# Performance work log

Hardware: AMD Instinct MI355X
Metric: run time of the kernel (lower is better)

The kernel has to match this reference:

```python
import jax, jax.numpy as jnp
import numpy as np

B, C, H, W = 32, 256, 56, 56
WS = 7            # window size (grid/dilated windows)
NH = 4            # num heads = C // dim_head
DH = 64           # dim_head
CMID = 256        # dim_mid = dim_in * exp_ratio
EPS = 1e-5


def _depthwise(x, w):
    # x: (b, C, h, w), w: (C, 1, k, k), 'same' padding, groups=C
    return jax.lax.conv_general_dilated(
        x, w, window_strides=(1, 1), padding='SAME',
        feature_group_count=x.shape[1],
        dimension_numbers=('NCHW', 'OIHW', 'NCHW'))


def setup_inputs() -> dict:
    key = jax.random.key(0)
    ks = jax.random.split(key, 12)
    return {
        'x': jax.random.normal(ks[0], (B, C, H, W), jnp.float32),
        'bn_gamma': jnp.ones((C,), jnp.float32),
        'bn_beta': jnp.zeros((C,), jnp.float32),
        'bn_mean': jnp.zeros((C,), jnp.float32),
        'bn_var': jnp.ones((C,), jnp.float32),
        'w_qk': jax.random.normal(ks[1], (2 * C, C), jnp.float32) * 0.05,
        'w_v': jax.random.normal(ks[2], (CMID, C), jnp.float32) * 0.05,
        'w_conv3': jax.random.normal(ks[3], (CMID, 1, 3, 3), jnp.float32) * 0.1,
        'w_conv5': jax.random.normal(ks[4], (CMID, 1, 5, 5), jnp.float32) * 0.1,
        'w_conv7': jax.random.normal(ks[5], (CMID, 1, 7, 7), jnp.float32) * 0.1,
        'attn_w': jax.random.uniform(ks[6], (1, CMID, 1, 1), jnp.float32),
        'c3_w': jax.random.uniform(ks[7], (1, CMID, 1, 1), jnp.float32),
        'c5_w': jax.random.uniform(ks[8], (1, CMID, 1, 1), jnp.float32),
        'c7_w': jax.random.uniform(ks[9], (1, CMID, 1, 1), jnp.float32),
        'w_proj': jax.random.normal(ks[10], (C, CMID), jnp.float32) * 0.05,
    }


def reference(x, bn_gamma, bn_beta, bn_mean, bn_var, w_qk, w_v,
              w_conv3, w_conv5, w_conv7, attn_w, c3_w, c5_w, c7_w, w_proj):
    shortcut = x
    # BatchNorm2d (eval mode, running stats)
    g = (bn_gamma / jnp.sqrt(bn_var + EPS))[None, :, None, None]
    x = (x - bn_mean[None, :, None, None]) * g + bn_beta[None, :, None, None]

    Bc, Cc, Hc, Wc = x.shape
    n1, n2 = Hc // WS, Wc // WS
    # grid/dilated windowing: 'b c (h1 n1) (w1 n2) -> (b n1 n2) c h1 w1'
    xw = (x.reshape(Bc, Cc, WS, n1, WS, n2)
           .transpose(0, 3, 5, 1, 2, 4)
           .reshape(Bc * n1 * n2, Cc, WS, WS))
    b = xw.shape[0]
    hw = WS * WS

    # qk 1x1 conv -> split into per-head q, k: (b, nh, hw, dh)
    qk = jnp.einsum('oc,bchw->bohw', w_qk, xw).reshape(b, 2, NH, DH, hw)
    q = qk[:, 0].transpose(0, 1, 3, 2)
    k = qk[:, 1].transpose(0, 1, 3, 2)

    # v 1x1 conv (attn_pre=False: attention over projected v)
    v = jnp.einsum('oc,bchw->bohw', w_v, xw)  # (b, CMID, ws, ws)
    vh = v.reshape(b, NH, CMID // NH, hw).transpose(0, 1, 3, 2)

    scale = 1.0 / jnp.sqrt(jnp.asarray(DH, x.dtype))
    attn = jax.nn.softmax(jnp.einsum('bnqd,bnkd->bnqk', q, k) * scale, axis=-1)
    x_spa = (jnp.einsum('bnqk,bnkd->bnqd', attn, vh)
             .transpose(0, 1, 3, 2).reshape(b, CMID, WS, WS))

    # multi-scale depthwise conv branch + weighted fusion + residual
    c3 = _depthwise(v, w_conv3)
    c5 = _depthwise(v, w_conv5)
    c7 = _depthwise(v, w_conv7)
    xc = x_spa * attn_w + c3 * c3_w + c5 * c5_w + c7 * c7_w + v

    # unwindow: '(b n1 n2) c h1 w1 -> b c (h1 n1) (w1 n2)'
    x = (xc.reshape(Bc, n1, n2, CMID, WS, WS)
           .transpose(0, 3, 4, 1, 5, 2)
           .reshape(Bc, CMID, Hc, Wc))

    # output 1x1 projection + residual (drop/drop_path are 0)
    x = jnp.einsum('oc,bchw->bohw', w_proj, x)
    return shortcut + x
```

## Files before the change

kernel.cpp:

```cpp
#include <hip/hip_runtime.h>
#include <cstddef>
#include <cstdint>

typedef short bf16x8 __attribute__((ext_vector_type(8)));
typedef float f32x4 __attribute__((ext_vector_type(4)));

#define MFMA16(a, b, c) __builtin_amdgcn_mfma_f32_16x16x32_bf16((a), (b), (c), 0, 0, 0)

__device__ __forceinline__ unsigned short f2bf(float f) {
  unsigned u = __float_as_uint(f);
  u = (u + 0x7FFFu + ((u >> 16) & 1u)) >> 16;
  return (unsigned short)u;
}
__device__ __forceinline__ float bf2f(unsigned short h) {
  return __uint_as_float(((unsigned)h) << 16);
}

__global__ void wprep(const float* __restrict__ bn_g, const float* __restrict__ bn_b,
                      const float* __restrict__ bn_m, const float* __restrict__ bn_v,
                      const float* __restrict__ w_qk, const float* __restrict__ w_v,
                      const float* __restrict__ w_proj,
                      const float* __restrict__ w3, const float* __restrict__ w5,
                      const float* __restrict__ w7,
                      unsigned short* __restrict__ Wqk, unsigned short* __restrict__ Wv,
                      unsigned short* __restrict__ Wp,
                      float* __restrict__ bqk, float* __restrict__ bv,
                      float* __restrict__ w3T, float* __restrict__ w5T,
                      float* __restrict__ w7T) {
  int blk = blockIdx.x, t = threadIdx.x;
  if (blk == 4) {
    for (int idx = t; idx < 21248; idx += 256) {
      if (idx < 2304) {
        int k2 = idx >> 8, c = idx & 255;
        w3T[idx] = w3[c * 9 + k2];
      } else if (idx < 8704) {
        int i = idx - 2304;
        int k2 = i >> 8, c = i & 255;
        w5T[i] = w5[c * 25 + k2];
      } else {
        int i = idx - 8704;
        int k2 = i >> 8, c = i & 255;
        w7T[i] = w7[c * 49 + k2];
      }
    }
    return;
  }
  int o = blk * 256 + t;
  if (o < 512) {
    float scale = (o < 256) ? 0.125f : 1.0f;
    float bias = 0.f;
    for (int c = 0; c < 256; ++c) {
      float g = bn_g[c] / sqrtf(bn_v[c] + 1e-5f);
      float be = bn_b[c] - bn_m[c] * g;
      float wv = w_qk[o * 256 + c];
      bias += wv * be;
      Wqk[o * 256 + c] = f2bf(wv * g * scale);
    }
    bqk[o] = bias * scale;
  } else if (o < 768) {
    int oo = o - 512;
    float bias = 0.f;
    for (int c = 0; c < 256; ++c) {
      float g = bn_g[c] / sqrtf(bn_v[c] + 1e-5f);
      float be = bn_b[c] - bn_m[c] * g;
      float wv = w_v[oo * 256 + c];
      bias += wv * be;
      Wv[oo * 256 + c] = f2bf(wv * g);
    }
    bv[oo] = bias;
  } else {
    int oo = o - 768;
    for (int c = 0; c < 256; ++c) Wp[oo * 256 + c] = f2bf(w_proj[oo * 256 + c]);
  }
}

__global__ __launch_bounds__(256) void xpose(const float* __restrict__ x,
                                             unsigned short* __restrict__ xT) {
  __shared__ float tile[64 * 68];
  int blk = blockIdx.x;
  int bb = blk / 196;
  int rem = blk - bb * 196;
  int cblk = rem / 49;
  int pblk = rem - cblk * 49;
  int t = threadIdx.x;
  {
    int r = t >> 2, seg = t & 3;
    const float* src = x + (size_t)bb * 802816 + (size_t)(cblk * 64 + r) * 3136 +
                       pblk * 64 + seg * 16;
    float4 v0 = ((const float4*)src)[0];
    float4 v1 = ((const float4*)src)[1];
    float4 v2 = ((const float4*)src)[2];
    float4 v3 = ((const float4*)src)[3];
    float* td = tile + r * 68 + seg * 16;
    td[0] = v0.x; td[1] = v0.y; td[2] = v0.z; td[3] = v0.w;
    td[4] = v1.x; td[5] = v1.y; td[6] = v1.z; td[7] = v1.w;
    td[8] = v2.x; td[9] = v2.y; td[10] = v2.z; td[11] = v2.w;
    td[12] = v3.x; td[13] = v3.y; td[14] = v3.z; td[15] = v3.w;
  }
  __syncthreads();
  {
    int p = t >> 2, cs = t & 3;
    alignas(16) unsigned short tmp[16];
#pragma unroll
    for (int u = 0; u < 16; ++u) tmp[u] = f2bf(tile[(cs * 16 + u) * 68 + p]);
    unsigned short* dst = xT + (size_t)(bb * 3136 + pblk * 64 + p) * 256 +
                          cblk * 64 + cs * 16;
    ((uint4*)dst)[0] = *(const uint4*)(tmp);
    ((uint4*)dst)[1] = *(const uint4*)(tmp + 8);
  }
}

__global__ __launch_bounds__(512, 2) void k2_win(
    const unsigned short* __restrict__ xT, const unsigned short* __restrict__ Wqk,
    const unsigned short* __restrict__ Wv, const float* __restrict__ bqk,
    const float* __restrict__ bv, const float* __restrict__ w3T,
    const float* __restrict__ w5T, const float* __restrict__ w7T,
    const float* __restrict__ aw, const float* __restrict__ c3w,
    const float* __restrict__ c5w, const float* __restrict__ c7w,
    unsigned short* __restrict__ xcT) {
  extern __shared__ char smem[];
  unsigned short* v_lds = (unsigned short*)smem;
  unsigned short* xw = (unsigned short*)(smem + 36864);
  unsigned short* q_lds = (unsigned short*)(smem + 62736);
  unsigned short* k_lds = (unsigned short*)(smem + 81168);
  unsigned short* Sb = (unsigned short*)(smem + 99600);
  float* spa = (float*)(smem + 118032);

  const int tid = threadIdx.x;
  const int l = tid & 63;
  const int w = tid >> 6;
  const int l15 = l & 15;
  const int lg = l >> 4;
  const int blk = blockIdx.x;
  const int bb = blk >> 6, i1 = (blk >> 3) & 7, i2 = blk & 7;

  for (int idx = tid; idx < 1568; idx += 512) {
    int r = idx >> 5, seg = idx & 31;
    int h1 = (r * 9363) >> 16;
    int w1 = r - h1 * 7;
    int pix = bb * 3136 + (h1 * 8 + i1) * 56 + w1 * 8 + i2;
    uint4 d = *(const uint4*)(xT + (size_t)pix * 256 + seg * 8);
    *(uint4*)(xw + r * 264 + seg * 8) = d;
  }
  __syncthreads();

  {
    f32x4 acc[2][4];
#pragma unroll
    for (int mf = 0; mf < 2; ++mf)
#pragma unroll
      for (int nt = 0; nt < 4; ++nt) acc[mf][nt] = (f32x4){0.f, 0.f, 0.f, 0.f};
#pragma unroll 2
    for (int ks = 0; ks < 8; ++ks) {
      bf16x8 a0 = *(const bf16x8*)(Wv + (w * 32 + l15) * 256 + ks * 32 + lg * 8);
      bf16x8 a1 = *(const bf16x8*)(Wv + (w * 32 + 16 + l15) * 256 + ks * 32 + lg * 8);
      bf16x8 b[4];
#pragma unroll
      for (int nt = 0; nt < 4; ++nt) {
        int j = nt * 16 + l15;
        if (j > 48) j = 48;
        b[nt] = *(const bf16x8*)(xw + j * 264 + ks * 32 + lg * 8);
      }
#pragma unroll
      for (int nt = 0; nt < 4; ++nt) {
        acc[0][nt] = MFMA16(a0, b[nt], acc[0][nt]);
        acc[1][nt] = MFMA16(a1, b[nt], acc[1][nt]);
      }
    }
#pragma unroll
    for (int mf = 0; mf < 2; ++mf)
#pragma unroll
      for (int ri = 0; ri < 4; ++ri) {
        int c = w * 32 + mf * 16 + lg * 4 + ri;
        float bvv = bv[c];
#pragma unroll
        for (int nt = 0; nt < 4; ++nt) {
          int p = nt * 16 + l15;
          v_lds[c * 72 + p] = f2bf(acc[mf][nt][ri] + bvv);
        }
      }
  }
  __syncthreads();

  for (int hp = 0; hp < 2; ++hp) {
    const int hs = w >> 2;
    const int sub = w & 3;
    const int h = hp * 2 + hs;

    {
      int obase = (sub < 2) ? (h * 64 + sub * 32) : (256 + h * 64 + (sub & 1) * 32);
      f32x4 acc[2][4];
#pragma unroll
      for (int mf = 0; mf < 2; ++mf)
#pragma unroll
        for (int nt = 0; nt < 4; ++nt) acc[mf][nt] = (f32x4){0.f, 0.f, 0.f, 0.f};
#pragma unroll 2
      for (int ks = 0; ks < 8; ++ks) {
        bf16x8 a0 = *(const bf16x8*)(Wqk + (obase + l15) * 256 + ks * 32 + lg * 8);
        bf16x8 a1 = *(const bf16x8*)(Wqk + (obase + 16 + l15) * 256 + ks * 32 + lg * 8);
        bf16x8 b[4];
#pragma unroll
        for (int nt = 0; nt < 4; ++nt) {
          int j = nt * 16 + l15;
          if (j > 48) j = 48;
          b[nt] = *(const bf16x8*)(xw + j * 264 + ks * 32 + lg * 8);
        }
#pragma unroll
        for (int nt = 0; nt < 4; ++nt) {
          acc[0][nt] = MFMA16(a0, b[nt], acc[0][nt]);
          acc[1][nt] = MFMA16(a1, b[nt], acc[1][nt]);
        }
      }
      unsigned short* dst = ((sub < 2) ? q_lds : k_lds) + hs * 4608;
      int dbase = (sub & 1) * 32;
#pragma unroll
      for (int mf = 0; mf < 2; ++mf)
#pragma unroll
        for (int ri = 0; ri < 4; ++ri) {
          float bias = bqk[obase + mf * 16 + lg * 4 + ri];
          int d = dbase + mf * 16 + lg * 4 + ri;
#pragma unroll
          for (int nt = 0; nt < 4; ++nt) {
            int p = nt * 16 + l15;
            dst[p * 72 + d] = f2bf(acc[mf][nt][ri] + bias);
          }
        }
    }
    __syncthreads();

    {
      f32x4 s[4];
#pragma unroll
      for (int nt = 0; nt < 4; ++nt) s[nt] = (f32x4){0.f, 0.f, 0.f, 0.f};
#pragma unroll
      for (int ks = 0; ks < 2; ++ks) {
        bf16x8 a = *(const bf16x8*)(q_lds + hs * 4608 + (sub * 16 + l15) * 72 +
                                    ks * 32 + lg * 8);
        bf16x8 b[4];
#pragma unroll
        for (int nt = 0; nt < 4; ++nt)
          b[nt] = *(const bf16x8*)(k_lds + hs * 4608 + (nt * 16 + l15) * 72 +
                                   ks * 32 + lg * 8);
#pragma unroll
        for (int nt = 0; nt < 4; ++nt) s[nt] = MFMA16(a, b[nt], s[nt]);
      }
#pragma unroll
      for (int ri = 0; ri < 4; ++ri) {
        float s0 = s[0][ri], s1 = s[1][ri], s2 = s[2][ri], s3v = s[3][ri];
        if (l15 != 0) s3v = -1e30f;
        float m = fmaxf(fmaxf(s0, s1), fmaxf(s2, s3v));
        m = fmaxf(m, __shfl_xor(m, 1));
        m = fmaxf(m, __shfl_xor(m, 2));
        m = fmaxf(m, __shfl_xor(m, 4));
        m = fmaxf(m, __shfl_xor(m, 8));
        float e0 = __expf(s0 - m), e1 = __expf(s1 - m);
        float e2 = __expf(s2 - m), e3 = __expf(s3v - m);
        float sum = e0 + e1 + e2 + e3;
        sum += __shfl_xor(sum, 1);
        sum += __shfl_xor(sum, 2);
        sum += __shfl_xor(sum, 4);
        sum += __shfl_xor(sum, 8);
        float inv = 1.f / sum;
        int row = sub * 16 + lg * 4 + ri;
        unsigned short* sb = Sb + hs * 4608 + row * 72 + l15;
        sb[0] = f2bf(e0 * inv);
        sb[16] = f2bf(e1 * inv);
        sb[32] = f2bf(e2 * inv);
        sb[48] = f2bf(e3 * inv);
      }
    }
    __syncthreads();

    {
      f32x4 acc[4];
#pragma unroll
      for (int nt = 0; nt < 4; ++nt) acc[nt] = (f32x4){0.f, 0.f, 0.f, 0.f};
#pragma unroll
      for (int ks = 0; ks < 2; ++ks) {
        bf16x8 a = *(const bf16x8*)(Sb + hs * 4608 + (sub * 16 + l15) * 72 +
                                    ks * 32 + lg * 8);
        bf16x8 b[4];
#pragma unroll
        for (int nt = 0; nt < 4; ++nt)
          b[nt] = *(const bf16x8*)(v_lds + (h * 64 + nt * 16 + l15) * 72 +
                                   ks * 32 + lg * 8);
#pragma unroll
        for (int nt = 0; nt < 4; ++nt) acc[nt] = MFMA16(a, b[nt], acc[nt]);
      }
#pragma unroll
      for (int nt = 0; nt < 4; ++nt)
#pragma unroll
        for (int ri = 0; ri < 4; ++ri) {
          int p = sub * 16 + lg * 4 + ri;
          if (p < 49) spa[hs * 3328 + (nt * 16 + l15) * 52 + p] = acc[nt][ri];
        }
    }
    __syncthreads();

    {
      int cl = ((w & 1) << 6) + l;
      int c = hp * 128 + cl;
      int hs2 = cl >> 6, dp = cl & 63;
      const float* spaC = spa + hs2 * 3328 + dp * 52;
      float awc = aw[c], c3c = c3w[c], c5c = c5w[c], c7c = c7w[c];
      float W3[9], W5[25], W7[49];
#pragma unroll
      for (int k2 = 0; k2 < 9; ++k2) W3[k2] = w3T[k2 * 256 + c];
#pragma unroll
      for (int k2 = 0; k2 < 25; ++k2) W5[k2] = w5T[k2 * 256 + c];
#pragma unroll
      for (int k2 = 0; k2 < 49; ++k2) W7[k2] = w7T[k2 * 256 + c];
#pragma unroll
      for (int pass = 0; pass < 2; ++pass) {
        int hr = (w >> 1) + pass * 4;
        if (hr <= 6) {
          float vr[7][7];
#pragma unroll
          for (int dy = -3; dy <= 3; ++dy) {
            int ry = hr + dy;
            if ((unsigned)ry < 7u) {
#pragma unroll
              for (int cc = 0; cc < 7; ++cc)
                vr[dy + 3][cc] = bf2f(v_lds[c * 72 + ry * 7 + cc]);
            }
          }
          float sp[7];
#pragma unroll
          for (int ww = 0; ww < 7; ++ww) sp[ww] = spaC[hr * 7 + ww];
#pragma unroll
          for (int ww = 0; ww < 7; ++ww) {
            float s3a = 0.f, s5a = 0.f, s7a = 0.f;
#pragma unroll
            for (int dy = -3; dy <= 3; ++dy) {
              if ((unsigned)(hr + dy) < 7u) {
#pragma unroll
                for (int dx = -3; dx <= 3; ++dx) {
                  int cc = ww + dx;
                  if (cc >= 0 && cc < 7) {
                    float vv = vr[dy + 3][cc];
                    s7a = fmaf(W7[(dy + 3) * 7 + dx + 3], vv, s7a);
                    if (dy >= -2 && dy <= 2 && dx >= -2 && dx <= 2)
                      s5a = fmaf(W5[(dy + 2) * 5 + dx + 2], vv, s5a);
                    if (dy >= -1 && dy <= 1 && dx >= -1 && dx <= 1)
                      s3a = fmaf(W3[(dy + 1) * 3 + dx + 1], vv, s3a);
                  }
                }
              }
            }
            float val = sp[ww] * awc + s3a * c3c + s5a * c5c + s7a * c7c + vr[3][ww];
            int pixp = bb * 3136 + (hr * 8 + i1) * 56 + ww * 8 + i2;
            xcT[(size_t)pixp * 256 + c] = f2bf(val);
          }
        }
      }
    }
    __syncthreads();
  }
}

__global__ __launch_bounds__(256) void k3_proj(const unsigned short* __restrict__ Wp,
                                               const unsigned short* __restrict__ xcT,
                                               const float* __restrict__ x,
                                               float* __restrict__ out) {
  const int tid = threadIdx.x, l = tid & 63, w = tid >> 6;
  const int l15 = l & 15, lg = l >> 4;
  const int blk = blockIdx.x;
  f32x4 acc[4][4];
#pragma unroll
  for (int mf = 0; mf < 4; ++mf)
#pragma unroll
    for (int nf = 0; nf < 4; ++nf) acc[mf][nf] = (f32x4){0.f, 0.f, 0.f, 0.f};
#pragma unroll 2
  for (int ks = 0; ks < 8; ++ks) {
    bf16x8 a[4], b[4];
#pragma unroll
    for (int mf = 0; mf < 4; ++mf)
      a[mf] = *(const bf16x8*)(Wp + (w * 64 + mf * 16 + l15) * 256 + ks * 32 + lg * 8);
#pragma unroll
    for (int nf = 0; nf < 4; ++nf)
      b[nf] = *(const bf16x8*)(xcT + (size_t)(blk * 64 + nf * 16 + l15) * 256 +
                               ks * 32 + lg * 8);
#pragma unroll
    for (int mf = 0; mf < 4; ++mf)
#pragma unroll
      for (int nf = 0; nf < 4; ++nf) acc[mf][nf] = MFMA16(a[mf], b[nf], acc[mf][nf]);
  }
  int bb = (blk * 64) / 3136;
  int loc0 = blk * 64 - bb * 3136;
#pragma unroll
  for (int mf = 0; mf < 4; ++mf)
#pragma unroll
    for (int nf = 0; nf < 4; ++nf)
#pragma unroll
      for (int ri = 0; ri < 4; ++ri) {
        int o = w * 64 + mf * 16 + lg * 4 + ri;
        int ploc = loc0 + nf * 16 + l15;
        size_t addr = (size_t)bb * 802816 + (size_t)o * 3136 + ploc;
        out[addr] = x[addr] + acc[mf][nf][ri];
      }
}

extern "C" void kernel_launch(void* const* d_in, const int* in_sizes, int n_in,
                              void* d_out, int out_size, void* d_ws, size_t ws_size,
                              hipStream_t stream) {
  const float* x = (const float*)d_in[0];
  const float* bn_g = (const float*)d_in[1];
  const float* bn_b = (const float*)d_in[2];
  const float* bn_m = (const float*)d_in[3];
  const float* bn_v = (const float*)d_in[4];
  const float* w_qk = (const float*)d_in[5];
  const float* w_v = (const float*)d_in[6];
  const float* w3 = (const float*)d_in[7];
  const float* w5 = (const float*)d_in[8];
  const float* w7 = (const float*)d_in[9];
  const float* aw = (const float*)d_in[10];
  const float* c3w = (const float*)d_in[11];
  const float* c5w = (const float*)d_in[12];
  const float* c7w = (const float*)d_in[13];
  const float* w_pr = (const float*)d_in[14];
  float* out = (float*)d_out;
  char* ws = (char*)d_ws;

  unsigned short* Wqk = (unsigned short*)ws;
  unsigned short* Wv = (unsigned short*)(ws + 262144);
  unsigned short* Wp = (unsigned short*)(ws + 393216);
  float* bqk = (float*)(ws + 524288);
  float* bv = (float*)(ws + 526336);
  float* w3T = (float*)(ws + 527360);
  float* w5T = (float*)(ws + 536576);
  float* w7T = (float*)(ws + 562176);
  unsigned short* xT = (unsigned short*)(ws + 1048576);
  unsigned short* xcT = (unsigned short*)(ws + 52428800);

  wprep<<<5, 256, 0, stream>>>(bn_g, bn_b, bn_m, bn_v, w_qk, w_v, w_pr, w3, w5, w7,
                               Wqk, Wv, Wp, bqk, bv, w3T, w5T, w7T);
  xpose<<<6272, 256, 0, stream>>>(x, xT);
  hipFuncSetAttribute(reinterpret_cast<const void*>(k2_win),
                      hipFuncAttributeMaxDynamicSharedMemorySize, 144656);
  k2_win<<<2048, 512, 144656, stream>>>(xT, Wqk, Wv, bqk, bv, w3T, w5T, w7T, aw, c3w,
                                        c5w, c7w, xcT);
  k3_proj<<<1568, 256, 0, stream>>>(Wp, xcT, x, out);
}
```

Before: 418.7 us.

## Process one head per iteration to shrink LDS and double k2 occupancy

Restructures the window kernel so each iteration handles one head. The V projection for that head is computed alongside Q/K in the same loop rather than as a separate full-width stage. This cuts dynamic shared memory from about 145 KB to about 74 KB and raises launch bounds to 4 blocks per SM, aiming for more resident waves to hide latency. In exchange there are more sequential barriers per block, and half the waves sit idle in the softmax stage and one wave in the depthwise stage. Register pressure under the tighter launch bound could cause spills in the depthwise-conv section.

```diff
diff --git a/kernel.cpp b/kernel.cpp
--- a/kernel.cpp
+++ b/kernel.cpp
@@ -110,7 +110,7 @@
   }
 }
 
-__global__ __launch_bounds__(512, 2) void k2_win(
+__global__ __launch_bounds__(512, 4) void k2_win(
     const unsigned short* __restrict__ xT, const unsigned short* __restrict__ Wqk,
     const unsigned short* __restrict__ Wv, const float* __restrict__ bqk,
     const float* __restrict__ bv, const float* __restrict__ w3T,
@@ -119,85 +119,41 @@
     const float* __restrict__ c5w, const float* __restrict__ c7w,
     unsigned short* __restrict__ xcT) {
   extern __shared__ char smem[];
-  unsigned short* v_lds = (unsigned short*)smem;
-  unsigned short* xw = (unsigned short*)(smem + 36864);
-  unsigned short* q_lds = (unsigned short*)(smem + 62736);
-  unsigned short* k_lds = (unsigned short*)(smem + 81168);
-  unsigned short* Sb = (unsigned short*)(smem + 99600);
-  float* spa = (float*)(smem + 118032);
+  unsigned short* xw = (unsigned short*)smem;
+  unsigned short* v_lds = (unsigned short*)(smem + 25872);
+  unsigned short* q_lds = (unsigned short*)(smem + 33152);
+  unsigned short* k_lds = (unsigned short*)(smem + 42368);
+  unsigned short* Sb = (unsigned short*)(smem + 51584);
+  float* spa = (float*)(smem + 60800);
 
   const int tid = threadIdx.x;
-  const int l = tid & 63;
-  const int w = tid >> 6;
-  const int l15 = l & 15;
-  const int lg = l >> 4;
+  const int l = tid & 63, w = tid >> 6, l15 = l & 15, lg = l >> 4;
   const int blk = blockIdx.x;
   const int bb = blk >> 6, i1 = (blk >> 3) & 7, i2 = blk & 7;
 
   for (int idx = tid; idx < 1568; idx += 512) {
     int r = idx >> 5, seg = idx & 31;
-    int h1 = (r * 9363) >> 16;
-    int w1 = r - h1 * 7;
+    int h1 = (r * 9363) >> 16, w1 = r - h1 * 7;
     int pix = bb * 3136 + (h1 * 8 + i1) * 56 + w1 * 8 + i2;
-    uint4 d = *(const uint4*)(xT + (size_t)pix * 256 + seg * 8);
-    *(uint4*)(xw + r * 264 + seg * 8) = d;
-  }
+    *(uint4*)(xw + r * 264 + seg * 8) =
+        *(const uint4*)(xT + (size_t)pix * 256 + seg * 8);
+  }
+  if (tid < 8) v_lds[64 * 56 + tid] = 0;
   __syncthreads();
 
-  {
-    f32x4 acc[2][4];
-#pragma unroll
-    for (int mf = 0; mf < 2; ++mf)
-#pragma unroll
-      for (int nt = 0; nt < 4; ++nt) acc[mf][nt] = (f32x4){0.f, 0.f, 0.f, 0.f};
-#pragma unroll 2
-    for (int ks = 0; ks < 8; ++ks) {
-      bf16x8 a0 = *(const bf16x8*)(Wv + (w * 32 + l15) * 256 + ks * 32 + lg * 8);
-      bf16x8 a1 = *(const bf16x8*)(Wv + (w * 32 + 16 + l15) * 256 + ks * 32 + lg * 8);
-      bf16x8 b[4];
+  for (int h = 0; h < 4; ++h) {
+    {
+      const bool isq = (w < 4);
+      const int wt = isq ? w : (w - 4);
+      const int obase = isq ? (h * 64 + wt * 16) : (256 + h * 64 + wt * 16);
+      f32x4 aq[4], av[4];
 #pragma unroll
       for (int nt = 0; nt < 4; ++nt) {
-        int j = nt * 16 + l15;
-        if (j > 48) j = 48;
-        b[nt] = *(const bf16x8*)(xw + j * 264 + ks * 32 + lg * 8);
-      }
-#pragma unroll
-      for (int nt = 0; nt < 4; ++nt) {
-        acc[0][nt] = MFMA16(a0, b[nt], acc[0][nt]);
-        acc[1][nt] = MFMA16(a1, b[nt], acc[1][nt]);
-      }
-    }
-#pragma unroll
-    for (int mf = 0; mf < 2; ++mf)
-#pragma unroll
-      for (int ri = 0; ri < 4; ++ri) {
-        int c = w * 32 + mf * 16 + lg * 4 + ri;
-        float bvv = bv[c];
-#pragma unroll
-        for (int nt = 0; nt < 4; ++nt) {
-          int p = nt * 16 + l15;
-          v_lds[c * 72 + p] = f2bf(acc[mf][nt][ri] + bvv);
-        }
-      }
-  }
-  __syncthreads();
-
-  for (int hp = 0; hp < 2; ++hp) {
-    const int hs = w >> 2;
-    const int sub = w & 3;
-    const int h = hp * 2 + hs;
-
-    {
-      int obase = (sub < 2) ? (h * 64 + sub * 32) : (256 + h * 64 + (sub & 1) * 32);
-      f32x4 acc[2][4];
-#pragma unroll
-      for (int mf = 0; mf < 2; ++mf)
-#pragma unroll
-        for (int nt = 0; nt < 4; ++nt) acc[mf][nt] = (f32x4){0.f, 0.f, 0.f, 0.f};
+        aq[nt] = (f32x4){0.f, 0.f, 0.f, 0.f};
+        av[nt] = (f32x4){0.f, 0.f, 0.f, 0.f};
+      }
 #pragma unroll 2
       for (int ks = 0; ks < 8; ++ks) {
-        bf16x8 a0 = *(const bf16x8*)(Wqk + (obase + l15) * 256 + ks * 32 + lg * 8);
-        bf16x8 a1 = *(const bf16x8*)(Wqk + (obase + 16 + l15) * 256 + ks * 32 + lg * 8);
         bf16x8 b[4];
 #pragma unroll
         for (int nt = 0; nt < 4; ++nt) {
@@ -205,64 +161,75 @@
           if (j > 48) j = 48;
           b[nt] = *(const bf16x8*)(xw + j * 264 + ks * 32 + lg * 8);
         }
+        bf16x8 a0 = *(const bf16x8*)(Wqk + (obase + l15) * 256 + ks * 32 + lg * 8);
+#pragma unroll
+        for (int nt = 0; nt < 4; ++nt) aq[nt] = MFMA16(a0, b[nt], aq[nt]);
+        if (isq) {
+          bf16x8 a1 =
+              *(const bf16x8*)(Wv + (h * 64 + wt * 16 + l15) * 256 + ks * 32 + lg * 8);
+#pragma unroll
+          for (int nt = 0; nt < 4; ++nt) av[nt] = MFMA16(a1, b[nt], av[nt]);
+        }
+      }
+      unsigned short* dst = isq ? q_lds : k_lds;
+#pragma unroll
+      for (int ri = 0; ri < 4; ++ri) {
+        float bias = bqk[obase + lg * 4 + ri];
+        int d = wt * 16 + lg * 4 + ri;
 #pragma unroll
         for (int nt = 0; nt < 4; ++nt) {
-          acc[0][nt] = MFMA16(a0, b[nt], acc[0][nt]);
-          acc[1][nt] = MFMA16(a1, b[nt], acc[1][nt]);
-        }
-      }
-      unsigned short* dst = ((sub < 2) ? q_lds : k_lds) + hs * 4608;
-      int dbase = (sub & 1) * 32;
-#pragma unroll
-      for (int mf = 0; mf < 2; ++mf)
+          int p = nt * 16 + l15;
+          dst[p * 72 + d] = f2bf(aq[nt][ri] + bias);
+        }
+      }
+      if (isq) {
 #pragma unroll
         for (int ri = 0; ri < 4; ++ri) {
-          float bias = bqk[obase + mf * 16 + lg * 4 + ri];
-          int d = dbase + mf * 16 + lg * 4 + ri;
+          int cl = wt * 16 + lg * 4 + ri;
+          float bvv = bv[h * 64 + cl];
 #pragma unroll
           for (int nt = 0; nt < 4; ++nt) {
             int p = nt * 16 + l15;
-            dst[p * 72 + d] = f2bf(acc[mf][nt][ri] + bias);
+            if (p < 56) v_lds[cl * 56 + p] = f2bf(av[nt][ri] + bvv);
           }
         }
+      }
     }
     __syncthreads();
 
-    {
+    if (w < 4) {
       f32x4 s[4];
 #pragma unroll
       for (int nt = 0; nt < 4; ++nt) s[nt] = (f32x4){0.f, 0.f, 0.f, 0.f};
 #pragma unroll
       for (int ks = 0; ks < 2; ++ks) {
-        bf16x8 a = *(const bf16x8*)(q_lds + hs * 4608 + (sub * 16 + l15) * 72 +
-                                    ks * 32 + lg * 8);
+        bf16x8 a = *(const bf16x8*)(q_lds + (w * 16 + l15) * 72 + ks * 32 + lg * 8);
         bf16x8 b[4];
 #pragma unroll
         for (int nt = 0; nt < 4; ++nt)
-          b[nt] = *(const bf16x8*)(k_lds + hs * 4608 + (nt * 16 + l15) * 72 +
-                                   ks * 32 + lg * 8);
+          b[nt] = *(const bf16x8*)(k_lds + (nt * 16 + l15) * 72 + ks * 32 + lg * 8);
 #pragma unroll
         for (int nt = 0; nt < 4; ++nt) s[nt] = MFMA16(a, b[nt], s[nt]);
       }
 #pragma unroll
       for (int ri = 0; ri < 4; ++ri) {
-        float s0 = s[0][ri], s1 = s[1][ri], s2 = s[2][ri], s3v = s[3][ri];
-        if (l15 != 0) s3v = -1e30f;
-        float m = fmaxf(fmaxf(s0, s1), fmaxf(s2, s3v));
+        float s0 = s[0][ri], s1 = s[1][ri], s2 = s[2][ri], s3 = s[3][ri];
+        if (l15 != 0) s3 = -1e30f;
+        float m = fmaxf(fmaxf(s0, s1), fmaxf(s2, s3));
         m = fmaxf(m, __shfl_xor(m, 1));
         m = fmaxf(m, __shfl_xor(m, 2));
         m = fmaxf(m, __shfl_xor(m, 4));
         m = fmaxf(m, __shfl_xor(m, 8));
         float e0 = __expf(s0 - m), e1 = __expf(s1 - m);
-        float e2 = __expf(s2 - m), e3 = __expf(s3v - m);
+        float e2 = __expf(s2 - m), e3 = __expf(s3 - m);
         float sum = e0 + e1 + e2 + e3;
         sum += __shfl_xor(sum, 1);
         sum += __shfl_xor(sum, 2);
         sum += __shfl_xor(sum, 4);
         sum += __shfl_xor(sum, 8);
         float inv = 1.f / sum;
-        int row = sub * 16 + lg * 4 + ri;
-        unsigned short* sb = Sb + hs * 4608 + row * 72 + l15;
+        int row = w * 16 + lg * 4 + ri;
+        unsigned short* sb = Sb + row * 72 + l15;
         sb[0] = f2bf(e0 * inv);
         sb[16] = f2bf(e1 * inv);
         sb[32] = f2bf(e2 * inv);
@@ -272,36 +239,37 @@
     __syncthreads();
 
     {
-      f32x4 acc[4];
-#pragma unroll
-      for (int nt = 0; nt < 4; ++nt) acc[nt] = (f32x4){0.f, 0.f, 0.f, 0.f};
+      int pr = w & 3, nc = (w >> 2) * 2;
+      f32x4 acc[2];
+      acc[0] = (f32x4){0.f, 0.f, 0.f, 0.f};
+      acc[1] = (f32x4){0.f, 0.f, 0.f, 0.f};
 #pragma unroll
       for (int ks = 0; ks < 2; ++ks) {
-        bf16x8 a = *(const bf16x8*)(Sb + hs * 4608 + (sub * 16 + l15) * 72 +
-                                    ks * 32 + lg * 8);
-        bf16x8 b[4];
-#pragma unroll
-        for (int nt = 0; nt < 4; ++nt)
-          b[nt] = *(const bf16x8*)(v_lds + (h * 64 + nt * 16 + l15) * 72 +
-                                   ks * 32 + lg * 8);
-#pragma unroll
-        for (int nt = 0; nt < 4; ++nt) acc[nt] = MFMA16(a, b[nt], acc[nt]);
-      }
-#pragma unroll
-      for (int nt = 0; nt < 4; ++nt)
+        bf16x8 a = *(const bf16x8*)(Sb + (pr * 16 + l15) * 72 + ks * 32 + lg * 8);
+#pragma unroll
+        for (int t = 0; t < 2; ++t) {
+          bf16x8 b = *(const bf16x8*)(v_lds + ((nc + t) * 16 + l15) * 56 +
+                                      ks * 32 + lg * 8);
+          acc[t] = MFMA16(a, b, acc[t]);
+        }
+      }
+#pragma unroll
+      for (int t = 0; t < 2; ++t) {
+        int cl = (nc + t) * 16 + l15;
 #pragma unroll
         for (int ri = 0; ri < 4; ++ri) {
-          int p = sub * 16 + lg * 4 + ri;
-          if (p < 49) spa[hs * 3328 + (nt * 16 + l15) * 52 + p] = acc[nt][ri];
-        }
+          int p = pr * 16 + lg * 4 + ri;
+          if (p < 49) spa[cl * 52 + p] = acc[t][ri];
+        }
+      }
     }
     __syncthreads();
 
-    {
-      int cl = ((w & 1) << 6) + l;
-      int c = hp * 128 + cl;
-      int hs2 = cl >> 6, dp = cl & 63;
-      const float* spaC = spa + hs2 * 3328 + dp * 52;
+    if (w < 7) {
+      int cl = l;
+      int c = h * 64 + cl;
+      int hr = w;
+      const float* spaC = spa + cl * 52;
       float awc = aw[c], c3c = c3w[c], c5c = c5w[c], c7c = c7w[c];
       float W3[9], W5[25], W7[49];
 #pragma unroll
@@ -310,48 +278,45 @@
       for (int k2 = 0; k2 < 25; ++k2) W5[k2] = w5T[k2 * 256 + c];
 #pragma unroll
       for (int k2 = 0; k2 < 49; ++k2) W7[k2] = w7T[k2 * 256 + c];
-#pragma unroll
-      for (int pass = 0; pass < 2; ++pass) {
-        int hr = (w >> 1) + pass * 4;
-        if (hr <= 6) {
-          float vr[7][7];
-#pragma unroll
-          for (int dy = -3; dy <= 3; ++dy) {
-            int ry = hr + dy;
-            if ((unsigned)ry < 7u) {
-#pragma unroll
-              for (int cc = 0; cc < 7; ++cc)
-                vr[dy + 3][cc] = bf2f(v_lds[c * 72 + ry * 7 + cc]);
+      float vr[7][7];
+#pragma unroll
+      for (int dy = -3; dy <= 3; ++dy) {
+        int ry = hr + dy;
+        if ((unsigned)ry < 7u) {
+#pragma unroll
+          for (int cc = 0; cc < 7; ++cc)
+            vr[dy + 3][cc] = bf2f(v_lds[cl * 56 + ry * 7 + cc]);
+        }
+      }
+      float sp[7];
+#pragma unroll
+      for (int ww = 0; ww < 7; ++ww) sp[ww] = spaC[hr * 7 + ww];
+#pragma unroll
+      for (int ww = 0; ww < 7; ++ww) {
+        float s3a = 0.f, s5a = 0.f, s7a = 0.f;
+#pragma unroll
+        for (int dy = -3; dy <= 3; ++dy) {
+          if ((unsigned)(hr + dy) < 7u) {
+#pragma unroll
+            for (int dx = -3; dx <= 3; ++dx) {
+              int cc = ww + dx;
+              if (cc >= 0 && cc < 7) {
+                float vv = vr[dy + 3][cc];
+                s7a = fmaf(W7[(dy + 3) * 7 + dx + 3], vv, s7a);
+                if (dy >= -2 && dy <= 2 && dx >= -2 && dx <= 2)
+                  s5a = fmaf(W5[(dy + 2) * 5 + dx + 2], vv, s5a);
+                if (dy >= -1 && dy <= 1 && dx >= -1 && dx <= 1)
+                  s3a = fmaf(W3[(dy + 1) * 3 + dx + 1], vv, s3a);
+              }
             }
           }
-          float sp[7];
-#pragma unroll
-          for (int ww = 0; ww < 7; ++ww) sp[ww] = spaC[hr * 7 + ww];
-#pragma unroll
-          for (int ww = 0; ww < 7; ++ww) {
-            float s3a = 0.f, s5a = 0.f, s7a = 0.f;
-#pragma unroll
-            for (int dy = -3; dy <= 3; ++dy) {
-              if ((unsigned)(hr + dy) < 7u) {
-#pragma unroll
-                for (int dx = -3; dx <= 3; ++dx) {
-                  int cc = ww + dx;
-                  if (cc >= 0 && cc < 7) {
-                    float vv = vr[dy + 3][cc];
-                    s7a = fmaf(W7[(dy + 3) * 7 + dx + 3], vv, s7a);
-                    if (dy >= -2 && dy <= 2 && dx >= -2 && dx <= 2)
-                      s5a = fmaf(W5[(dy + 2) * 5 + dx + 2], vv, s5a);
-                    if (dy >= -1 && dy <= 1 && dx >= -1 && dx <= 1)
-                      s3a = fmaf(W3[(dy + 1) * 3 + dx + 1], vv, s3a);
-                  }
-                }
-              }
-            }
-            float val = sp[ww] * awc + s3a * c3c + s5a * c5c + s7a * c7c + vr[3][ww];
-            int pixp = bb * 3136 + (hr * 8 + i1) * 56 + ww * 8 + i2;
-            xcT[(size_t)pixp * 256 + c] = f2bf(val);
-          }
-        }
+        }
+        float val = fmaf(sp[ww], awc,
+                    fmaf(s3a, c3c,
+                    fmaf(s5a, c5c,
+                    fmaf(s7a, c7c, vr[3][ww]))));
+        int pixp = bb * 3136 + (hr * 8 + i1) * 56 + ww * 8 + i2;
+        xcT[(size_t)pixp * 256 + c] = f2bf(val);
       }
     }
     __syncthreads();
@@ -436,8 +401,8 @@
                                Wqk, Wv, Wp, bqk, bv, w3T, w5T, w7T);
   xpose<<<6272, 256, 0, stream>>>(x, xT);
   hipFuncSetAttribute(reinterpret_cast<const void*>(k2_win),
-                      hipFuncAttributeMaxDynamicSharedMemorySize, 144656);
-  k2_win<<<2048, 512, 144656, stream>>>(xT, Wqk, Wv, bqk, bv, w3T, w5T, w7T, aw, c3w,
-                                        c5w, c7w, xcT);
+                      hipFuncAttributeMaxDynamicSharedMemorySize, 74112);
+  k2_win<<<2048, 512, 74112, stream>>>(xT, Wqk, Wv, bqk, bv, w3T, w5T, w7T, aw, c3w,
+                                       c5w, c7w, xcT);
   k3_proj<<<1568, 256, 0, stream>>>(Wp, xcT, x, out);
 }
```

Result: slower. 1.075 ms (+156.8%).
